# Kernel optimization log

Measured on AMD Instinct MI355X. Metric: run time of the kernel, lower is better.

Reference implementation:

```python
import jax, jax.numpy as jnp
import numpy as np

# SSD post-process constants (mirror torch module init args)
V0, V1 = 0.1, 0.2            # box coder variances
SCORE_THRESH = 0.05
NMS_THRESH = 0.45
DET_PER_IMG = 100
MIN_SIZE = 0.01
PRE_NMS_TOPK = 1000          # padded candidate budget for jit-safe NMS


def setup_inputs() -> dict:
    key = jax.random.key(0)
    k1, k2, k3 = jax.random.split(key, 3)
    B, P, C = 32, 24564, 81
    pred_logits = jax.random.normal(k1, (B, P, C), dtype=jnp.float32)
    pred_boxes = jax.random.normal(k2, (B, P, 4), dtype=jnp.float32)
    # priors in (cx, cy, w, h), normalized coords
    u = jax.random.uniform(k3, (P, 4), dtype=jnp.float32)
    priors = jnp.concatenate([u[:, :2], 0.02 + 0.3 * u[:, 2:]], axis=-1)
    target_sizes = 512.0 * jnp.ones((B, 2), dtype=jnp.float32)  # (h, w)
    return {"pred_logits": pred_logits, "pred_boxes": pred_boxes,
            "priors": priors, "target_sizes": target_sizes}


def _decode(rel, priors):
    # SSD box decode: priors are cxcywh, rel codes scaled by variances -> xyxy
    xy = priors[:, :2] + rel[:, :2] * V0 * priors[:, 2:]
    wh = priors[:, 2:] * jnp.exp(rel[:, 2:] * V1)
    return jnp.concatenate([xy - wh / 2, xy + wh / 2], axis=-1)


def _box_iou(a, b):
    area_a = (a[:, 2] - a[:, 0]) * (a[:, 3] - a[:, 1])
    area_b = (b[:, 2] - b[:, 0]) * (b[:, 3] - b[:, 1])
    lt = jnp.maximum(a[:, None, :2], b[None, :, :2])
    rb = jnp.minimum(a[:, None, 2:], b[None, :, 2:])
    wh = jnp.clip(rb - lt, 0.0)
    inter = wh[..., 0] * wh[..., 1]
    return inter / (area_a[:, None] + area_b[None, :] - inter + 1e-12)


def _per_image(logits, rel, priors, tsize):
    P, C = logits.shape
    boxes = _decode(rel, priors)                       # [P,4] xyxy
    scale = jnp.tile(tsize[::-1], 2)                   # (w,h,w,h) = flip(0).repeat(2)
    boxes = boxes * scale
    scores = jax.nn.softmax(logits, axis=-1)[:, 1:]    # drop background, [P,C-1]
    size_ok = ((boxes[:, 2] - boxes[:, 0]) >= MIN_SIZE) & \
              ((boxes[:, 3] - boxes[:, 1]) >= MIN_SIZE)
    masked = jnp.where((scores > SCORE_THRESH) & size_ok[:, None], scores, -1.0)
    top_s, top_i = jax.lax.top_k(masked.reshape(-1), PRE_NMS_TOPK)
    prior_i = top_i // (C - 1)
    cls0 = top_i % (C - 1)                             # label - 1
    b = boxes[prior_i]                                 # [K,4]
    valid = top_s > SCORE_THRESH
    # batched_nms: offset boxes by class so different classes never overlap
    maxc = jnp.max(jnp.where(valid[:, None], b, 0.0))
    bo = b + (cls0.astype(b.dtype) * (maxc + 1.0))[:, None]
    ious = jax.lax.stop_gradient(_box_iou(bo, bo))
    K = PRE_NMS_TOPK
    idx = jnp.arange(K)

    def body(i, keep):
        sup = jnp.any(keep & (idx < i) & (ious[i] > NMS_THRESH))
        return keep.at[i].set(keep[i] & ~sup)

    keep = jax.lax.fori_loop(0, K, body, valid)
    kept_s = jnp.where(keep, top_s, -1.0)
    fs, fi = jax.lax.top_k(kept_s, DET_PER_IMG)        # keep order == score order
    fb = b[fi]
    fl = cls0[fi] + 1
    fvalid = fs > SCORE_THRESH
    fb = jnp.where(fvalid[:, None], fb, 0.0)
    fl = jnp.where(fvalid, fl, -1)
    fs = jnp.where(fvalid, fs, 0.0)
    return fb, fs, fl, fvalid


def reference(pred_logits, pred_boxes, priors, target_sizes):
    # Returns padded per-image detections: boxes [B,100,4], scores [B,100],
    # labels [B,100] (int, -1 = padding), valid mask [B,100].
    return jax.vmap(_per_image, in_axes=(0, 0, None, 0))(
        pred_logits, pred_boxes, priors, target_sizes)
```

## Files before the change

### kernel.cpp

```cpp
#include <hip/hip_runtime.h>
#include <stdint.h>

typedef unsigned int u32;
typedef unsigned long long u64;
typedef long long i64;

#define NCLS 81
#define KTOP 1000
#define DETS 100
#define CANDCAP 2048
#define BIGCAP 131072
#define TPB 256
#define RCH 64
#define NCH 4
#define CNT_STRIDE 32
#define FBINS 4096

__device__ __forceinline__ double exp_ref(double x)
{
    const double LOG2E = 1.4426950408889634074;
    const double LN2HI = 6.93147180369123816490e-01;
    const double LN2LO = 1.90821492927058770002e-10;
    double nf = rint(x * LOG2E);
    int n = (int)nf;
    double r = fma(-nf, LN2HI, x);
    r = fma(-nf, LN2LO, r);
    double p = 2.0876756987868099e-09;
    p = fma(p, r, 2.5052108385441720e-08);
    p = fma(p, r, 2.7557319223985891e-07);
    p = fma(p, r, 2.7557319223985893e-06);
    p = fma(p, r, 2.4801587301587302e-05);
    p = fma(p, r, 1.9841269841269841e-04);
    p = fma(p, r, 1.3888888888888889e-03);
    p = fma(p, r, 8.3333333333333332e-03);
    p = fma(p, r, 4.1666666666666664e-02);
    p = fma(p, r, 1.6666666666666666e-01);
    p = fma(p, r, 5.0000000000000000e-01);
    p = fma(p, r, 1.0);
    p = fma(p, r, 1.0);
    i64 bits = ((i64)(n + 1023)) << 52;
    return p * __longlong_as_double(bits);
}

__device__ __forceinline__ double fexp(double x, const double* __restrict__ etab)
{
    const double L32     = 1.4426950408889634074 * 32.0;
    const double LN32HI  = 6.93147180369123816490e-01 / 32.0;
    const double LN32LO  = 1.90821492927058770002e-10 / 32.0;
    double nf = rint(x * L32);
    int n = (int)nf;
    double r = fma(-nf, LN32HI, x);
    r = fma(-nf, LN32LO, r);
    double p = 4.1666666666666664e-02;
    p = fma(p, r, 1.6666666666666666e-01);
    p = fma(p, r, 5.0000000000000000e-01);
    p = fma(p, r, 1.0);
    p = fma(p, r, 1.0);
    double tb = etab[n & 31];
    i64 q = (i64)(n >> 5) + 1023;
    return (p * tb) * __longlong_as_double(q << 52);
}

__global__ __launch_bounds__(TPB)
void score_kernel(const float* __restrict__ logits, const float* __restrict__ rel,
                  const float* __restrict__ priors, const float* __restrict__ ts,
                  int P, u64* __restrict__ bigCand, u32* __restrict__ bigCnt)
{
    __shared__ float xs[RCH * NCLS];
    __shared__ double etab[32];
    __shared__ double sden[RCH];
    __shared__ float tfl[RCH];
    __shared__ u32 okm[RCH];
    __shared__ u32 wsum[4];
    __shared__ u32 s_base;
    int img = blockIdx.y;
    int p0 = blockIdx.x * TPB;
    int tid = threadIdx.x;
    int lane = tid & 63, wid = tid >> 6;
    int sub = tid & 3;
    int rloc = tid >> 2;

    if (tid < 32)
        etab[tid] = exp_ref((double)tid * (6.93147180369123816490e-01 / 32.0));

    for (int ch = 0; ch < NCH; ++ch) {
        int rbase = p0 + ch * RCH;
        __syncthreads();
        int nrows = min(RCH, P - rbase);
        if (nrows == RCH) {
            const float4* s4 = (const float4*)(logits + ((size_t)img * P + rbase) * NCLS);
            float4* d4 = (float4*)xs;
#pragma unroll
            for (int k = 0; k < 5; ++k) d4[k * TPB + tid] = s4[k * TPB + tid];
            if (tid < 16) d4[5 * TPB + tid] = s4[5 * TPB + tid];
        } else if (nrows > 0) {
            const float* s1 = logits + ((size_t)img * P + rbase) * NCLS;
            int nflat = nrows * NCLS;
            for (int f = tid; f < nflat; f += TPB) xs[f] = s1[f];
        }
        __syncthreads();

        int p = rbase + rloc;
        bool live = (p < P);
        const float* row = xs + rloc * NCLS;

        float vals[21];
#pragma unroll
        for (int i = 0; i < 21; ++i) {
            int j = sub + 4 * i;
            vals[i] = (live && j < NCLS) ? row[j] : -1.0e30f;
        }

        float m = vals[0];
#pragma unroll
        for (int i = 1; i < 21; ++i) m = fmaxf(m, vals[i]);
        m = fmaxf(m, __shfl_xor(m, 1));
        m = fmaxf(m, __shfl_xor(m, 2));

        double md = (double)m;
        double acc = 0.0;
#pragma unroll
        for (int i = 0; i < 21; ++i) {
            if (vals[i] > -1.0e29f)
                acc += fexp((double)vals[i] - md, etab);
        }
        acc += __shfl_xor(acc, 1);
        acc += __shfl_xor(acc, 2);
        double s = acc;
        if (sub == 0) sden[rloc] = s;
        __syncthreads();

        if (tid < RCH) {
            int p2 = rbase + tid;
            bool ok2 = false;
            float t2 = 3.4e38f;
            if (p2 < P) {
                double s2 = sden[tid];
                t2 = logf(0.05f * (float)s2) - 3e-4f;
                const float* rp = rel + ((size_t)img * P + p2) * 4;
                const float* pp = priors + (size_t)p2 * 4;
                double pw = pp[2], ph = pp[3];
                double cx = (double)pp[0] + (double)rp[0] * 0.1 * pw;
                double cy = (double)pp[1] + (double)rp[1] * 0.1 * ph;
                double bw = pw * fexp((double)rp[2] * 0.2, etab);
                double bh = ph * fexp((double)rp[3] * 0.2, etab);
                double sw = (double)ts[img * 2 + 1], sh = (double)ts[img * 2 + 0];
                double x1 = (cx - bw * 0.5) * sw, x2 = (cx + bw * 0.5) * sw;
                double y1 = (cy - bh * 0.5) * sh, y2 = (cy + bh * 0.5) * sh;
                ok2 = (x2 - x1 >= 0.01) && (y2 - y1 >= 0.01);
            }
            okm[tid] = ok2 ? 1u : 0u;
            tfl[tid] = t2;
        }
        __syncthreads();
        bool ok = okm[rloc] != 0;
        float tf_lo = tfl[rloc];

        u32 cnt = 0;
#pragma unroll
        for (int i = 0; i < 21; ++i) {
            int j = sub + 4 * i;
            if (ok && j != 0 && vals[i] - m > tf_lo) cnt++;
        }
        u32 inc = cnt;
        for (int off = 1; off < 64; off <<= 1) {
            u32 v = __shfl_up(inc, off);
            if (lane >= off) inc += v;
        }
        if (lane == 63) wsum[wid] = inc;
        __syncthreads();
        if (tid == 0) {
            u32 tot = wsum[0] + wsum[1] + wsum[2] + wsum[3];
            s_base = tot ? atomicAdd(&bigCnt[(size_t)img * CNT_STRIDE], tot) : 0u;
        }
        __syncthreads();
        if (ok && cnt) {
            u32 wbase = 0;
            for (int w = 0; w < wid; ++w) wbase += wsum[w];
            u32 pos = s_base + wbase + inc - cnt;
#pragma unroll
            for (int i = 0; i < 21; ++i) {
                int j = sub + 4 * i;
                if (j != 0 && vals[i] - m > tf_lo) {
                    double e = fexp((double)vals[i] - md, etab);
                    double sc = e / s;
                    u64 entry = 0ULL;
                    if (sc > 0.05) {
                        u32 key = __float_as_uint((float)sc) ^ 0x80000000u;
                        u32 idx = (u32)p * 80u + (u32)(j - 1);
                        entry = ((u64)key << 32) | (u64)(u32)(~idx);
                    }
                    if (pos < BIGCAP)
                        bigCand[(size_t)img * BIGCAP + pos] = entry;
                    pos++;
                }
            }
        }
    }
}

__global__ __launch_bounds__(1024)
void select_nms_kernel(const u64* __restrict__ bigCand, const u32* __restrict__ bigCnt,
                       const float* __restrict__ rel, const float* __restrict__ priors,
                       const float* __restrict__ ts, int P,
                       float* __restrict__ out, int B)
{
    __shared__ u64 smemU[7584];
    __shared__ u64 supW16[16];
    __shared__ u32 s_sel, s_run, s_floor, s_cnt;
    __shared__ int s_i, s_t;
    int img = blockIdx.x;
    int tid = threadIdx.x;
    int lane = tid & 63;
    int wv = tid >> 6;
    u32 bc = bigCnt[(size_t)img * CNT_STRIDE];
    if (bc > (u32)BIGCAP) bc = BIGCAP;
    const u64* src = bigCand + (size_t)img * BIGCAP;

    u64* s    = smemU;
    u32* h    = (u32*)((char*)smemU + 16384);
    u32* tsum = (u32*)((char*)smemU + 32768);

    for (int i = tid; i < FBINS; i += 1024) h[i] = 0;
    if (tid == 0) { s_cnt = 0; s_t = -1; }
    __syncthreads();
    for (u32 k = tid; k < bc; k += 1024) {
        u32 key = (u32)(src[k] >> 32);
        if (key) atomicAdd(&h[key >> 20], 1u);
    }
    __syncthreads();
    tsum[tid] = h[tid * 4] + h[tid * 4 + 1] + h[tid * 4 + 2] + h[tid * 4 + 3];
    __syncthreads();
    for (int off = 1; off < 1024; off <<= 1) {
        u32 v = (tid + off < 1024) ? tsum[tid + off] : 0u;
        __syncthreads();
        tsum[tid] += v;
        __syncthreads();
    }
    if (tsum[tid] >= KTOP) atomicMax(&s_t, tid);
    __syncthreads();
    int t_star = s_t;
    if (t_star >= 0) {
        if (tid == t_star) {
            u32 run = (t_star + 1 < 1024) ? tsum[t_star + 1] : 0u;
            int d = 4 * t_star + 3;
            for (; d >= 4 * t_star; --d) {
                if (run + h[d] >= KTOP) break;
                run += h[d];
            }
            s_sel = (u32)d;
            s_run = run;
        }
    } else {
        if (tid == 0) s_sel = 0xFFFFFFFFu;
    }
    __syncthreads();
    u32 d12 = s_sel;
    if ((int)d12 >= 0) {
        u32 run0 = s_run;
        if (tid < 16) h[tid] = 0;
        __syncthreads();
        for (u32 k = tid; k < bc; k += 1024) {
            u32 key = (u32)(src[k] >> 32);
            if (key && (key >> 20) == d12) atomicAdd(&h[(key >> 16) & 0xF], 1u);
        }
        __syncthreads();
        if (tid == 0) {
            u32 run = run0;
            int b = 15;
            for (; b >= 0; --b) {
                run += h[b];
                if (run >= KTOP) break;
            }
            if (b < 0) b = 0;
            s_floor = ((d12 << 4) | (u32)b) << 16;
        }
    } else {
        if (tid == 0) s_floor = 0u;
    }
    __syncthreads();
    u32 fkey = s_floor;
    for (u32 k0 = 0; k0 < bc; k0 += 1024) {
        u32 k = k0 + tid;
        u64 e = 0; bool pass = false;
        if (k < bc) {
            e = src[k];
            u32 ky = (u32)(e >> 32);
            pass = ky && (ky >= fkey);
        }
        u64 mask = __ballot(pass);
        if (mask) {
            int leader = __ffsll((long long)mask) - 1;
            u32 basePos = 0;
            if (lane == leader) basePos = atomicAdd(&s_cnt, (u32)__popcll(mask));
            basePos = __shfl(basePos, leader);
            if (pass) {
                u32 pos = basePos + (u32)__popcll(mask & ((1ULL << lane) - 1ULL));
                if (pos < CANDCAP) s[pos] = e;
            }
        }
    }
    __syncthreads();
    u32 n = s_cnt; if (n > CANDCAP) n = CANDCAP;
    for (int k = tid; k < CANDCAP; k += 1024)
        if ((u32)k >= n) s[k] = 0ULL;
    __syncthreads();
    for (u32 len = 2; len <= CANDCAP; len <<= 1) {
        for (u32 j = len >> 1; j > 0; j >>= 1) {
            for (int i = tid; i < CANDCAP; i += 1024) {
                u32 ixj = (u32)i ^ j;
                if (ixj > (u32)i) {
                    u64 a = s[i], b = s[ixj];
                    bool up = ((i & len) == 0);
                    if (up ? (a < b) : (a > b)) { s[i] = b; s[ixj] = a; }
                }
            }
            __syncthreads();
        }
    }

    u64 e = (tid < KTOP) ? s[tid] : 0ULL;
    __syncthreads();

    double* o0   = (double*)smemU;
    double* o1   = (double*)((char*)smemU +  8000);
    double* o2   = (double*)((char*)smemU + 16000);
    double* o3   = (double*)((char*)smemU + 24000);
    double* arA  = (double*)((char*)smemU + 32000);
    int*    clsA = (int*)   ((char*)smemU + 44000);
    float*  scA  = (float*) ((char*)smemU + 48000);
    int*    keptS= (int*)   ((char*)smemU + 52000);
    double* red  = (double*)((char*)smemU + 52416);

    double b0 = 0, b1 = 0, b2 = 0, b3 = 0;
    int cls = 0;
    float score = -1.0f;
    bool validE = (tid < KTOP) && ((e >> 32) != 0ULL);
    double v = -1e300;
    if (tid < KTOP) {
        if (validE) {
            u32 key = (u32)(e >> 32);
            score = __uint_as_float(key ^ 0x80000000u);
            u32 idx = ~((u32)e);
            int p = (int)(idx / 80u), c0 = (int)(idx % 80u);
            cls = c0;
            const float* rp = rel + ((size_t)img * P + p) * 4;
            const float* pp = priors + (size_t)p * 4;
            double pw = pp[2], ph = pp[3];
            double cx = (double)pp[0] + (double)rp[0] * 0.1 * pw;
            double cy = (double)pp[1] + (double)rp[1] * 0.1 * ph;
            double bw = pw * exp_ref((double)rp[2] * 0.2);
            double bh = ph * exp_ref((double)rp[3] * 0.2);
            double sw = (double)ts[img * 2 + 1], sh = (double)ts[img * 2 + 0];
            b0 = (cx - bw * 0.5) * sw; b1 = (cy - bh * 0.5) * sh;
            b2 = (cx + bw * 0.5) * sw; b3 = (cy + bh * 0.5) * sh;
            v = fmax(fmax(b0, b1), fmax(b2, b3));
        } else {
            v = 0.0;
        }
        o0[tid] = b0; o1[tid] = b1; o2[tid] = b2; o3[tid] = b3;
        clsA[tid] = cls; scA[tid] = score;
        red[tid] = v;
    } else {
        red[tid] = -1e300;
    }
    __syncthreads();
    for (int off = 512; off > 0; off >>= 1) {
        if (tid < off) red[tid] = fmax(red[tid], red[tid + off]);
        __syncthreads();
    }
    double maxc1 = red[0] + 1.0;
    if (tid < KTOP) {
        double off_ = (double)cls * maxc1;
        double a0 = b0 + off_, a1 = b1 + off_, a2 = b2 + off_, a3 = b3 + off_;
        arA[tid] = (a2 - a0) * (a3 - a1);
    }
    u64 wb = __ballot(validE);
    if (lane == 0) supW16[wv] = wb;
    __syncthreads();
    u64 aliveW = (tid < 16) ? supW16[tid] : 0ULL;

    int cnt = 0;
    while (cnt < DETS) {
        if (wv == 0) {
            bool has = (lane < 16) && (aliveW != 0ULL);
            u64 bal = __ballot(has);
            int ni = -1;
            if (bal) {
                int w0 = __ffsll((i64)bal) - 1;
                u64 word = __shfl(aliveW, w0);
                int bt = __ffsll((i64)word) - 1;
                ni = w0 * 64 + bt;
            }
            if (lane == 0) s_i = ni;
        }
        __syncthreads();
        int i = s_i;
        if (i < 0) break;
        if (tid == 0) keptS[cnt] = i;
        cnt++;
        double offi = (double)clsA[i] * maxc1;
        double a0 = o0[i] + offi, a1 = o1[i] + offi;
        double a2 = o2[i] + offi, a3 = o3[i] + offi;
        double aA = arA[i];
        bool sup = false;
        if (tid < KTOP && tid > i) {
            double offj = (double)clsA[tid] * maxc1;
            double c0 = o0[tid] + offj, c1 = o1[tid] + offj;
            double c2 = o2[tid] + offj, c3 = o3[tid] + offj;
            double ltx = fmax(a0, c0), lty = fmax(a1, c1);
            double rbx = fmin(a2, c2), rby = fmin(a3, c3);
            double wx = fmax(rbx - ltx, 0.0), wy = fmax(rby - lty, 0.0);
            double inter = wx * wy;
            sup = inter > 0.45 * (((aA + arA[tid]) - inter) + 1e-12);
        }
        u64 ws = __ballot(sup);
        if (lane == 0) supW16[wv] = ws;
        __syncthreads();
        if (tid < 16) {
            aliveW &= ~supW16[tid];
            if (tid == (i >> 6)) aliveW &= ~(1ULL << (i & 63));
        }
    }
    __syncthreads();

    int r = tid;
    if (r < DETS) {
        float f0 = 0.f, f1 = 0.f, f2 = 0.f, f3 = 0.f, sc = 0.f, lb = -1.0f, vd = 0.f;
        if (r < cnt) {
            int i2 = keptS[r];
            f0 = (float)o0[i2]; f1 = (float)o1[i2];
            f2 = (float)o2[i2]; f3 = (float)o3[i2];
            sc = scA[i2];
            lb = (float)(clsA[i2] + 1);
            vd = 1.0f;
        }
        ((float4*)out)[(size_t)img * DETS + r] = make_float4(f0, f1, f2, f3);
        out[(size_t)B * 400 + (size_t)img * DETS + r] = sc;
        out[(size_t)B * 500 + (size_t)img * DETS + r] = lb;
        out[(size_t)B * 600 + (size_t)img * DETS + r] = vd;
    }
}

extern "C" void kernel_launch(void* const* d_in, const int* in_sizes, int n_in,
                              void* d_out, int out_size, void* d_ws, size_t ws_size,
                              hipStream_t stream)
{
    const float* logits = (const float*)d_in[0];
    const float* rel    = (const float*)d_in[1];
    const float* priors = (const float*)d_in[2];
    const float* ts     = (const float*)d_in[3];
    float* out = (float*)d_out;
    int P = in_sizes[2] / 4;
    int B = in_sizes[3] / 2;

    char* ws = (char*)d_ws;
    size_t zero_bytes = (size_t)B * CNT_STRIDE * 4;
    size_t o_big = (zero_bytes + 255) & ~(size_t)255;

    u32* bigCnt  = (u32*)ws;
    u64* bigCand = (u64*)(ws + o_big);

    hipMemsetAsync(ws, 0, zero_bytes, stream);

    dim3 g1((P + TPB - 1) / TPB, B);
    score_kernel<<<g1, TPB, 0, stream>>>(logits, rel, priors, ts, P, bigCand, bigCnt);
    select_nms_kernel<<<B, 1024, 0, stream>>>(bigCand, bigCnt, rel, priors, ts, P,
                                              out, B);
    (void)n_in; (void)out_size; (void)ws_size;
}
```

Measured before the change: 293.9 us.

## Split select/NMS into two kernels and fast-path few-candidate rows in scoring

The fused select+NMS kernel becomes two kernels, selectA (top-k selection, box decode, max-coordinate reduction) and nms_kernel, which pass decoded boxes, classes, scores and validity through global workspace. This frees the large shared-memory union for NMS and lets each kernel size its shared memory separately, at the cost of an extra launch and a global round trip. In score_kernel, padding lanes now hold -64 instead of -1e30, which drops the per-element branch in the softmax sum. Rows with at most three passing classes cache their values and indices so the emission step skips the 21-iteration rescan.

```diff
diff --git a/kernel.cpp b/kernel.cpp
--- a/kernel.cpp
+++ b/kernel.cpp
@@ -108,7 +108,7 @@
 #pragma unroll
         for (int i = 0; i < 21; ++i) {
             int j = sub + 4 * i;
-            vals[i] = (live && j < NCLS) ? row[j] : -1.0e30f;
+            vals[i] = (live && j < NCLS) ? row[j] : -64.0f;
         }
 
         float m = vals[0];
@@ -120,10 +120,8 @@
         double md = (double)m;
         double acc = 0.0;
 #pragma unroll
-        for (int i = 0; i < 21; ++i) {
-            if (vals[i] > -1.0e29f)
-                acc += fexp((double)vals[i] - md, etab);
-        }
+        for (int i = 0; i < 21; ++i)
+            acc += fexp((double)vals[i] - md, etab);
         acc += __shfl_xor(acc, 1);
         acc += __shfl_xor(acc, 2);
         double s = acc;
@@ -157,10 +155,18 @@
         float tf_lo = tfl[rloc];
 
         u32 cnt = 0;
+        float pv0 = 0.f, pv1 = 0.f, pv2 = 0.f;
+        int   pj0 = 0,   pj1 = 0,   pj2 = 0;
 #pragma unroll
         for (int i = 0; i < 21; ++i) {
             int j = sub + 4 * i;
-            if (ok && j != 0 && vals[i] - m > tf_lo) cnt++;
+            bool pass = ok && (j != 0) && (vals[i] - m > tf_lo);
+            if (pass) {
+                if (cnt == 0)      { pv0 = vals[i]; pj0 = j; }
+                else if (cnt == 1) { pv1 = vals[i]; pj1 = j; }
+                else if (cnt == 2) { pv2 = vals[i]; pj2 = j; }
+                cnt++;
+            }
         }
         u32 inc = cnt;
         for (int off = 1; off < 64; off <<= 1) {
@@ -178,41 +184,80 @@
             u32 wbase = 0;
             for (int w = 0; w < wid; ++w) wbase += wsum[w];
             u32 pos = s_base + wbase + inc - cnt;
-#pragma unroll
-            for (int i = 0; i < 21; ++i) {
-                int j = sub + 4 * i;
-                if (j != 0 && vals[i] - m > tf_lo) {
-                    double e = fexp((double)vals[i] - md, etab);
+            u64* dst = bigCand + (size_t)img * BIGCAP;
+            if (cnt <= 3) {
+                {
+                    double e = fexp((double)pv0 - md, etab);
                     double sc = e / s;
                     u64 entry = 0ULL;
                     if (sc > 0.05) {
                         u32 key = __float_as_uint((float)sc) ^ 0x80000000u;
-                        u32 idx = (u32)p * 80u + (u32)(j - 1);
+                        u32 idx = (u32)p * 80u + (u32)(pj0 - 1);
                         entry = ((u64)key << 32) | (u64)(u32)(~idx);
                     }
-                    if (pos < BIGCAP)
-                        bigCand[(size_t)img * BIGCAP + pos] = entry;
+                    if (pos < BIGCAP) dst[pos] = entry;
                     pos++;
                 }
+                if (cnt >= 2) {
+                    double e = fexp((double)pv1 - md, etab);
+                    double sc = e / s;
+                    u64 entry = 0ULL;
+                    if (sc > 0.05) {
+                        u32 key = __float_as_uint((float)sc) ^ 0x80000000u;
+                        u32 idx = (u32)p * 80u + (u32)(pj1 - 1);
+                        entry = ((u64)key << 32) | (u64)(u32)(~idx);
+                    }
+                    if (pos < BIGCAP) dst[pos] = entry;
+                    pos++;
+                }
+                if (cnt >= 3) {
+                    double e = fexp((double)pv2 - md, etab);
+                    double sc = e / s;
+                    u64 entry = 0ULL;
+                    if (sc > 0.05) {
+                        u32 key = __float_as_uint((float)sc) ^ 0x80000000u;
+                        u32 idx = (u32)p * 80u + (u32)(pj2 - 1);
+                        entry = ((u64)key << 32) | (u64)(u32)(~idx);
+                    }
+                    if (pos < BIGCAP) dst[pos] = entry;
+                    pos++;
+                }
+            } else {
+#pragma unroll
+                for (int i = 0; i < 21; ++i) {
+                    int j = sub + 4 * i;
+                    if (j != 0 && vals[i] - m > tf_lo) {
+                        double e = fexp((double)vals[i] - md, etab);
+                        double sc = e / s;
+                        u64 entry = 0ULL;
+                        if (sc > 0.05) {
+                            u32 key = __float_as_uint((float)sc) ^ 0x80000000u;
+                            u32 idx = (u32)p * 80u + (u32)(j - 1);
+                            entry = ((u64)key << 32) | (u64)(u32)(~idx);
+                        }
+                        if (pos < BIGCAP) dst[pos] = entry;
+                        pos++;
+                    }
+                }
             }
         }
     }
 }
 
 __global__ __launch_bounds__(1024)
-void select_nms_kernel(const u64* __restrict__ bigCand, const u32* __restrict__ bigCnt,
-                       const float* __restrict__ rel, const float* __restrict__ priors,
-                       const float* __restrict__ ts, int P,
-                       float* __restrict__ out, int B)
+void selectA_kernel(const u64* __restrict__ bigCand, const u32* __restrict__ bigCnt,
+                    const float* __restrict__ rel, const float* __restrict__ priors,
+                    const float* __restrict__ ts, int P,
+                    double* __restrict__ selD, int* __restrict__ clsG,
+                    float* __restrict__ scG, u32* __restrict__ valG,
+                    double* __restrict__ maxcG)
 {
     __shared__ u64 smemU[7584];
-    __shared__ u64 supW16[16];
     __shared__ u32 s_sel, s_run, s_floor, s_cnt;
-    __shared__ int s_i, s_t;
+    __shared__ int s_t;
     int img = blockIdx.x;
     int tid = threadIdx.x;
     int lane = tid & 63;
-    int wv = tid >> 6;
     u32 bc = bigCnt[(size_t)img * CNT_STRIDE];
     if (bc > (u32)BIGCAP) bc = BIGCAP;
     const u64* src = bigCand + (size_t)img * BIGCAP;
@@ -319,24 +364,14 @@
         }
     }
 
+    double* red = (double*)((char*)smemU + 16384);
     u64 e = (tid < KTOP) ? s[tid] : 0ULL;
-    __syncthreads();
-
-    double* o0   = (double*)smemU;
-    double* o1   = (double*)((char*)smemU +  8000);
-    double* o2   = (double*)((char*)smemU + 16000);
-    double* o3   = (double*)((char*)smemU + 24000);
-    double* arA  = (double*)((char*)smemU + 32000);
-    int*    clsA = (int*)   ((char*)smemU + 44000);
-    float*  scA  = (float*) ((char*)smemU + 48000);
-    int*    keptS= (int*)   ((char*)smemU + 52000);
-    double* red  = (double*)((char*)smemU + 52416);
-
     double b0 = 0, b1 = 0, b2 = 0, b3 = 0;
     int cls = 0;
     float score = -1.0f;
     bool validE = (tid < KTOP) && ((e >> 32) != 0ULL);
     double v = -1e300;
+    size_t ob = (size_t)img * 5000;
     if (tid < KTOP) {
         if (validE) {
             u32 key = (u32)(e >> 32);
@@ -358,22 +393,56 @@
         } else {
             v = 0.0;
         }
-        o0[tid] = b0; o1[tid] = b1; o2[tid] = b2; o3[tid] = b3;
-        clsA[tid] = cls; scA[tid] = score;
-        red[tid] = v;
-    } else {
-        red[tid] = -1e300;
-    }
+        selD[ob + tid]        = b0;
+        selD[ob + 1000 + tid] = b1;
+        selD[ob + 2000 + tid] = b2;
+        selD[ob + 3000 + tid] = b3;
+        clsG[(size_t)img * 1000 + tid] = cls;
+        scG[(size_t)img * 1000 + tid]  = score;
+        valG[(size_t)img * 1000 + tid] = validE ? 1u : 0u;
+    }
+    red[tid] = v;
     __syncthreads();
     for (int off = 512; off > 0; off >>= 1) {
         if (tid < off) red[tid] = fmax(red[tid], red[tid + off]);
         __syncthreads();
     }
     double maxc1 = red[0] + 1.0;
+    if (tid == 0) maxcG[img] = maxc1;
     if (tid < KTOP) {
         double off_ = (double)cls * maxc1;
         double a0 = b0 + off_, a1 = b1 + off_, a2 = b2 + off_, a3 = b3 + off_;
-        arA[tid] = (a2 - a0) * (a3 - a1);
+        selD[ob + 4000 + tid] = (a2 - a0) * (a3 - a1);
+    }
+}
+
+__global__ __launch_bounds__(1024)
+void nms_kernel(const double* __restrict__ selD, const int* __restrict__ clsG,
+                const float* __restrict__ scG, const u32* __restrict__ valG,
+                const double* __restrict__ maxcG, float* __restrict__ out, int B)
+{
+    __shared__ double o0[KTOP], o1[KTOP], o2[KTOP], o3[KTOP], arA[KTOP];
+    __shared__ int clsA[KTOP];
+    __shared__ float scA[KTOP];
+    __shared__ int keptS[DETS];
+    __shared__ u64 supW16[16];
+    __shared__ int s_i;
+    int img = blockIdx.x;
+    int tid = threadIdx.x;
+    int lane = tid & 63;
+    int wv = tid >> 6;
+    size_t ob = (size_t)img * 5000;
+    double maxc1 = maxcG[img];
+    bool validE = false;
+    if (tid < KTOP) {
+        o0[tid]  = selD[ob + tid];
+        o1[tid]  = selD[ob + 1000 + tid];
+        o2[tid]  = selD[ob + 2000 + tid];
+        o3[tid]  = selD[ob + 3000 + tid];
+        arA[tid] = selD[ob + 4000 + tid];
+        clsA[tid] = clsG[(size_t)img * 1000 + tid];
+        scA[tid]  = scG[(size_t)img * 1000 + tid];
+        validE = valG[(size_t)img * 1000 + tid] != 0;
     }
     u64 wb = __ballot(validE);
     if (lane == 0) supW16[wv] = wb;
@@ -456,16 +525,27 @@
 
     char* ws = (char*)d_ws;
     size_t zero_bytes = (size_t)B * CNT_STRIDE * 4;
-    size_t o_big = (zero_bytes + 255) & ~(size_t)255;
-
-    u32* bigCnt  = (u32*)ws;
-    u64* bigCand = (u64*)(ws + o_big);
+    size_t o_selD = (zero_bytes + 255) & ~(size_t)255;
+    size_t o_cls  = o_selD + (size_t)B * 5000 * 8;
+    size_t o_sc   = o_cls + (size_t)B * 1000 * 4;
+    size_t o_val  = o_sc + (size_t)B * 1000 * 4;
+    size_t o_maxc = o_val + (size_t)B * 1000 * 4;
+    size_t o_big  = (o_maxc + (size_t)B * 8 + 255) & ~(size_t)255;
+
+    u32* bigCnt   = (u32*)ws;
+    double* selD  = (double*)(ws + o_selD);
+    int* clsG     = (int*)(ws + o_cls);
+    float* scG    = (float*)(ws + o_sc);
+    u32* valG     = (u32*)(ws + o_val);
+    double* maxcG = (double*)(ws + o_maxc);
+    u64* bigCand  = (u64*)(ws + o_big);
 
     hipMemsetAsync(ws, 0, zero_bytes, stream);
 
     dim3 g1((P + TPB - 1) / TPB, B);
     score_kernel<<<g1, TPB, 0, stream>>>(logits, rel, priors, ts, P, bigCand, bigCnt);
-    select_nms_kernel<<<B, 1024, 0, stream>>>(bigCand, bigCnt, rel, priors, ts, P,
-                                              out, B);
+    selectA_kernel<<<B, 1024, 0, stream>>>(bigCand, bigCnt, rel, priors, ts, P,
+                                           selD, clsG, scG, valG, maxcG);
+    nms_kernel<<<B, 1024, 0, stream>>>(selD, clsG, scG, valG, maxcG, out, B);
     (void)n_in; (void)out_size; (void)ws_size;
 }
```

Measured after the change: 312.7 us. 1.06x slower.
